# Kernel tuning notes

Hardware: AMD Instinct MI355X
Metric: run time of the kernel (lower is better)

The kernel has to match this reference:

```python
import jax, jax.numpy as jnp
import numpy as np

H, NH, L, S, B, V = 512, 8, 6, 2048, 2, 32000
DH = H // NH
EPS = 1e-5


def posenc(h, s):
    pos = jnp.arange(s, dtype=jnp.float32)[:, None]
    div = jnp.power(10000.0, jnp.arange(0, h, 2, dtype=jnp.float32) / h)
    pe = jnp.zeros((s, h), dtype=jnp.float32)
    pe = pe.at[:, 0::2].set(jnp.sin(pos / div))
    pe = pe.at[:, 1::2].set(jnp.cos(pos / div))
    return pe


def layernorm(x, g, b):
    mu = jnp.mean(x, axis=-1, keepdims=True)
    var = jnp.mean(jnp.square(x - mu), axis=-1, keepdims=True)
    return (x - mu) * jax.lax.rsqrt(var + EPS) * g + b


def setup_inputs() -> dict:
    key = jax.random.key(0)
    ks = jax.random.split(key, 16)
    sc = 0.02
    return {
        "src": jax.random.randint(ks[0], (B, S), 0, V),
        "mask": jnp.ones((B, 1, 1, S), dtype=jnp.int32),
        "emb": jax.random.normal(ks[1], (V, H), jnp.float32) * sc,
        "Wq": jax.random.normal(ks[2], (L, H, H), jnp.float32) * sc,
        "bq": jnp.zeros((L, H), jnp.float32),
        "Wk": jax.random.normal(ks[3], (L, H, H), jnp.float32) * sc,
        "bk": jnp.zeros((L, H), jnp.float32),
        "Wv": jax.random.normal(ks[4], (L, H, H), jnp.float32) * sc,
        "bv": jnp.zeros((L, H), jnp.float32),
        "Wo": jax.random.normal(ks[5], (L, H, H), jnp.float32) * sc,
        "bo": jnp.zeros((L, H), jnp.float32),
        "gamma": jnp.ones((L, H), jnp.float32),
        "beta": jnp.zeros((L, H), jnp.float32),
        "W1": jax.random.normal(ks[6], (L, H, 4 * H), jnp.float32) * sc,
        "b1": jnp.zeros((L, 4 * H), jnp.float32),
        "W2": jax.random.normal(ks[7], (L, 4 * H, H), jnp.float32) * sc,
        "b2": jnp.zeros((L, H), jnp.float32),
    }


def reference(src, mask, emb, Wq, bq, Wk, bk, Wv, bv, Wo, bo, gamma, beta, W1, b1, W2, b2):
    x = emb[src] + posenc(H, S)[None, :, :]  # [B,S,H]
    for i in range(L):
        q = (x @ Wq[i] + bq[i]).reshape(B, S, NH, DH).transpose(0, 2, 1, 3)
        k = (x @ Wk[i] + bk[i]).reshape(B, S, NH, DH).transpose(0, 2, 1, 3)
        v = (x @ Wv[i] + bv[i]).reshape(B, S, NH, DH).transpose(0, 2, 1, 3)
        scores = jnp.einsum("bhqd,bhkd->bhqk", q, k) / jnp.sqrt(jnp.float32(DH))
        scores = jnp.where(mask == 0, jnp.float32(-1e20), scores)
        attn = jax.nn.softmax(scores, axis=-1)
        av = jnp.einsum("bhqk,bhkd->bhqd", attn, v)
        attn_out = av.transpose(0, 2, 1, 3).reshape(B, S, H) @ Wo[i] + bo[i]
        # NOTE: same LayerNorm params applied to both sublayers (as in source)
        res = x + layernorm(attn_out, gamma[i], beta[i])
        ffn = jax.nn.relu(res @ W1[i] + b1[i]) @ W2[i] + b2[i]
        x = res + layernorm(ffn, gamma[i], beta[i])
    return x
```

## Files before the change

### kernel.cpp

```cpp
#include <hip/hip_runtime.h>
#include <math.h>

#define HDIM 512
#define NHEAD 8
#define NLAYER 6
#define SEQ 2048
#define BATCH 2
#define DHEAD 64
#define TOKENS (BATCH*SEQ)
#define FFND (4*HDIM)
#define QSTR 1536

typedef unsigned short u16;
typedef unsigned long long u64;
typedef __attribute__((ext_vector_type(8))) short short8;
typedef __attribute__((ext_vector_type(4))) float f32x4;

__device__ __forceinline__ u16 f2b(float f) {
  unsigned u = __float_as_uint(f);
  u += 0x7FFFu + ((u >> 16) & 1u);
  return (u16)(u >> 16);
}

__device__ __forceinline__ unsigned cvtpk_bf16(float lo, float hi) {
  unsigned r;
  asm("v_cvt_pk_bf16_f32 %0, %1, %2" : "=v"(r) : "v"(lo), "v"(hi));
  return r;
}

__device__ __forceinline__ void gload_lds16(const u16* g, u16* l) {
  __builtin_amdgcn_global_load_lds((const __attribute__((address_space(1))) void*)g,
                                   (__attribute__((address_space(3))) void*)l, 16, 0, 0);
}

__global__ void embed_pe(const int* __restrict__ src, const float* __restrict__ emb,
                         float* __restrict__ X, u16* __restrict__ Xb) {
  int tok = blockIdx.x;
  int lane = threadIdx.x;
  int s = tok & (SEQ - 1);
  int c0 = lane * 8;
  const float* e = emb + (long)src[tok] * HDIM + c0;
  float v[8];
#pragma unroll
  for (int j = 0; j < 8; j++) {
    int c = c0 + j;
    float arg = (float)s * exp2f(-(float)(c & ~1) * 0.02595256917f);
    v[j] = e[j] + ((c & 1) ? cosf(arg) : sinf(arg));
  }
  float* xp = X + (long)tok * HDIM + c0;
#pragma unroll
  for (int j = 0; j < 8; j++) xp[j] = v[j];
  u16 hb[8];
#pragma unroll
  for (int j = 0; j < 8; j++) hb[j] = f2b(v[j]);
  uint4 pk;
  pk.x = hb[0] | ((unsigned)hb[1] << 16);
  pk.y = hb[2] | ((unsigned)hb[3] << 16);
  pk.z = hb[4] | ((unsigned)hb[5] << 16);
  pk.w = hb[6] | ((unsigned)hb[7] << 16);
  *(uint4*)(Xb + (long)tok * HDIM + c0) = pk;
}

__global__ void maskprep(const int* __restrict__ mask, u64* __restrict__ mb) {
  int t = threadIdx.x;
  int b = t >> 5, tile = t & 31;
  const int* m = mask + b * SEQ + tile * 64;
  u64 w = 0;
#pragma unroll
  for (int j = 0; j < 64; j++) w |= (u64)(m[j] != 0) << j;
  mb[t] = w;
}

__global__ __launch_bounds__(256) void prep_weights(
    const float* __restrict__ Wq, const float* __restrict__ Wk, const float* __restrict__ Wv,
    const float* __restrict__ Wo, const float* __restrict__ W1, const float* __restrict__ W2,
    const float* __restrict__ bq, const float* __restrict__ bk, const float* __restrict__ bv,
    u16* __restrict__ Wqkvt, u16* __restrict__ Wot, u16* __restrict__ W1t, u16* __restrict__ W2t,
    float* __restrict__ bqkv) {
  int t = blockIdx.x;
  int tid = threadIdx.x;
  if (t == 768) {
    for (int i = tid; i < 1536; i += 256)
      bqkv[i] = (i < 512) ? bq[i] : (i < 1024) ? bk[i - 512] : bv[i - 1024];
    return;
  }
  const float* src; u16* dst; int K, N, kt, nt; long drow0 = 0;
  if (t < 192)      { int m = t / 64, r = t % 64; src = (m==0)?Wq:(m==1)?Wk:Wv; dst = Wqkvt; drow0 = (long)m*512; K=512;  N=512;  kt=r/8;  nt=r%8; }
  else if (t < 256) { int r = t - 192; src = Wo; dst = Wot; K=512;  N=512;  kt=r/8;  nt=r%8; }
  else if (t < 512) { int r = t - 256; src = W1; dst = W1t; K=512;  N=2048; kt=r/32; nt=r%32; }
  else              { int r = t - 512; src = W2; dst = W2t; K=2048; N=512;  kt=r/8;  nt=r%8; }
  __shared__ __align__(16) u16 Lt[64 * 72];
  int kl = tid >> 2;
#pragma unroll
  for (int rr = 0; rr < 4; rr++) {
    int cl = (tid & 3) * 4 + rr * 16;
    float4 v = *(const float4*)(src + (long)(kt * 64 + kl) * N + nt * 64 + cl);
    Lt[(cl + 0) * 72 + kl] = f2b(v.x);
    Lt[(cl + 1) * 72 + kl] = f2b(v.y);
    Lt[(cl + 2) * 72 + kl] = f2b(v.z);
    Lt[(cl + 3) * 72 + kl] = f2b(v.w);
  }
  __syncthreads();
  int nl = tid >> 2;
  int kc = (tid & 3) * 16;
  u16* dp = dst + (drow0 + nt * 64 + nl) * (long)K + kt * 64 + kc;
  *(uint4*)dp       = *(const uint4*)&Lt[nl * 72 + kc];
  *(uint4*)(dp + 8) = *(const uint4*)&Lt[nl * 72 + kc + 8];
}

__global__ __launch_bounds__(256) void vtranspose(const u16* __restrict__ QKV,
                                                  u16* __restrict__ Vtb) {
  __shared__ __align__(16) u16 Lt[64 * 72];
  int tid = threadIdx.x;
  int bh = blockIdx.y, b = bh >> 3, h = bh & 7;
  int s0 = blockIdx.x * 64;
  const u16* vsrc = QKV + (long)(b * SEQ + s0) * QSTR + 1024 + h * DHEAD;
  int key = tid >> 2, dc = (tid & 3) * 16;
  const u16* vp = vsrc + (long)key * QSTR + dc;
  uint4 v0 = *(const uint4*)vp;
  uint4 v1 = *(const uint4*)(vp + 8);
  unsigned vr[8] = { v0.x, v0.y, v0.z, v0.w, v1.x, v1.y, v1.z, v1.w };
#pragma unroll
  for (int j = 0; j < 8; j++) {
    Lt[(dc + 2 * j) * 72 + key]     = (u16)vr[j];
    Lt[(dc + 2 * j + 1) * 72 + key] = (u16)(vr[j] >> 16);
  }
  __syncthreads();
  int d = tid >> 2, kc = (tid & 3) * 16;
  u16* dst = Vtb + ((long)bh * DHEAD + d) * SEQ + s0 + kc;
  *(uint4*)dst       = *(const uint4*)&Lt[d * 72 + kc];
  *(uint4*)(dst + 8) = *(const uint4*)&Lt[d * 72 + kc + 8];
}

template <int BN, int KSPLIT, bool RELU, bool WF32, bool WB16>
__global__ __launch_bounds__(256) void gemm_tn(const u16* __restrict__ A,
                                               const u16* __restrict__ Bt,
                                               const float* __restrict__ bias,
                                               float* __restrict__ Cf,
                                               u16* __restrict__ Cb,
                                               int M, int N, int K) {
  constexpr int NF = BN / 32;
  __shared__ __align__(16) u16 As[2][128 * 32];
  __shared__ __align__(16) u16 Bs[2][BN * 32];
  int tid = threadIdx.x;
  int wave = tid >> 6, lane = tid & 63;
  int ln = lane & 15, hi = lane >> 4;
  int wm = wave >> 1, wn = wave & 1;
  int m0 = blockIdx.y * 128, n0 = blockIdx.x * BN;
  int z = (KSPLIT > 1) ? blockIdx.z : 0;
  int Ks = K / KSPLIT;
  const u16* Ab = A + z * Ks;
  const u16* Bb = Bt + z * Ks;

  f32x4 acc[4][NF] = {};

  int srow = lane >> 2;
  int skc  = (lane & 3) * 8;

  auto issue = [&](int kt, int buf) {
    int k0 = kt * 32;
#pragma unroll
    for (int j = 0; j < 2; j++) {
      int row = (wave * 2 + j) * 16 + srow;
      gload_lds16(Ab + (long)(m0 + row) * K + k0 + skc, &As[buf][row * 32 + skc]);
    }
#pragma unroll
    for (int j = 0; j < BN / 64; j++) {
      int row = (wave * (BN / 64) + j) * 16 + srow;
      gload_lds16(Bb + (long)(n0 + row) * K + k0 + skc, &Bs[buf][row * 32 + skc]);
    }
  };

  int NT = Ks / 32;
  issue(0, 0);
  __syncthreads();
  for (int kt = 0; kt < NT; kt++) {
    int buf = kt & 1;
    if (kt + 1 < NT) issue(kt + 1, buf ^ 1);
    short8 af[4], bf[NF];
#pragma unroll
    for (int mt = 0; mt < 4; mt++)
      af[mt] = *(const short8*)&As[buf][(wm * 64 + mt * 16 + ln) * 32 + 8 * hi];
#pragma unroll
    for (int nt = 0; nt < NF; nt++)
      bf[nt] = *(const short8*)&Bs[buf][(wn * (BN / 2) + nt * 16 + ln) * 32 + 8 * hi];
#pragma unroll
    for (int mt = 0; mt < 4; mt++)
#pragma unroll
      for (int nt = 0; nt < NF; nt++)
        acc[mt][nt] = __builtin_amdgcn_mfma_f32_16x16x32_bf16(af[mt], bf[nt], acc[mt][nt], 0, 0, 0);
    __syncthreads();
  }

  float* Cz = WF32 ? (Cf + (long)z * M * N) : nullptr;
#pragma unroll
  for (int mt = 0; mt < 4; mt++)
#pragma unroll
    for (int nt = 0; nt < NF; nt++)
#pragma unroll
      for (int r = 0; r < 4; r++) {
        int row = m0 + wm * 64 + mt * 16 + hi * 4 + r;
        int col = n0 + wn * (BN / 2) + nt * 16 + ln;
        float v = acc[mt][nt][r];
        if (KSPLIT == 1 || z == 0) v += bias[col];
        if (RELU) v = fmaxf(v, 0.0f);
        if (WF32) Cz[(long)row * N + col] = v;
        if (WB16) Cb[(long)row * N + col] = f2b(v);
      }
}

__global__ __launch_bounds__(256) void attention(const u16* __restrict__ QKV,
                                                 const u16* __restrict__ Vtb,
                                                 const u64* __restrict__ maskb,
                                                 u16* __restrict__ Og) {
  __shared__ __align__(16) u16 Ks[2][64 * 64];
  __shared__ __align__(16) u16 Vs[2][64 * 64];
  __shared__ u64 Msk[SEQ / 64];
  int tid = threadIdx.x, w = tid >> 6, lane = tid & 63;
  int ln = lane & 15, hi = lane >> 4;
  int h0 = hi & 1, h1 = hi >> 1, ln7 = ln & 7;
  int lin = blockIdx.x;
  int lid = (lin & 7) * 64 + (lin >> 3);
  int bh = lid >> 5, qt = lid & 31;
  int b = bh >> 3, h = bh & 7;
  int q0 = qt * 64 + w * 16;
  const u16* qbase = QKV + (long)b * SEQ * QSTR + h * DHEAD;
  const u16* kbase = qbase + 512;
  const u16* vtbase = Vtb + (long)bh * DHEAD * SEQ;

  short8 qf[2];
#pragma unroll
  for (int ks = 0; ks < 2; ks++)
    qf[ks] = *(const short8*)(qbase + (long)(q0 + ln) * QSTR + ks * 32 + 8 * hi);

  u64 mw0 = 0;
  if (tid < SEQ / 64) mw0 = maskb[b * (SEQ / 64) + tid];

  int sr0 = tid >> 3, sc = tid & 7;
  const u16 *kp0, *kp1, *vp0, *vp1;
  {
    int r1 = sr0 + 32;
    int key0 = (sr0 & 7) | ((sr0 & 0x18) << 1) | ((sr0 & 0x20) >> 2);
    int key1 = (r1 & 7) | ((r1 & 0x18) << 1) | ((r1 & 0x20) >> 2);
    kp0 = kbase + (long)key0 * QSTR + (sc ^ (sr0 & 7)) * 8;
    kp1 = kbase + (long)key1 * QSTR + (sc ^ (r1 & 7)) * 8;
    vp0 = vtbase + (long)sr0 * SEQ + (sc ^ (sr0 & 7)) * 8;
    vp1 = vtbase + (long)r1 * SEQ + (sc ^ (r1 & 7)) * 8;
  }
  int d0 = sr0 * 64 + sc * 8, d1 = d0 + 2048;

  auto issue = [&](int t, int buf) {
    long ko = (long)t * (64 * QSTR);
    int vo = t * 64;
    gload_lds16(kp0 + ko, &Ks[buf][d0]);
    gload_lds16(kp1 + ko, &Ks[buf][d1]);
    gload_lds16(vp0 + vo, &Vs[buf][d0]);
    gload_lds16(vp1 + vo, &Vs[buf][d1]);
  };

  f32x4 o[4] = {};
  float lsum = 0.0f;
  const int NT = SEQ / 64;

  issue(0, 0);
  issue(1, 1);
  if (tid < SEQ / 64) Msk[tid] = mw0;
  asm volatile("s_waitcnt vmcnt(4)" ::: "memory");
  __builtin_amdgcn_sched_barrier(0);
  __builtin_amdgcn_s_barrier();
  __builtin_amdgcn_sched_barrier(0);

  for (int t = 0; t < NT; t++) {
    int buf = t & 1;
    u64 mw = Msk[t];

    f32x4 s[4] = {};
#pragma unroll
    for (int ks = 0; ks < 2; ks++)
#pragma unroll
      for (int kb = 0; kb < 4; kb++) {
        short8 kf = *(const short8*)&Ks[buf][(kb * 16 + ln) * 64 + (((ks << 2) + hi) ^ ln7) * 8];
        s[kb] = __builtin_amdgcn_mfma_f32_16x16x32_bf16(kf, qf[ks], s[kb], 0, 0, 0);
      }

    unsigned D[4][2];
    if (mw == 0xFFFFFFFFFFFFFFFFull) {
#pragma unroll
      for (int kb = 0; kb < 4; kb++) {
        float p[4];
#pragma unroll
        for (int r = 0; r < 4; r++) {
          float pv = __expf(s[kb][r] * 0.125f);
          lsum += pv;
          p[r] = pv;
        }
        D[kb][0] = cvtpk_bf16(p[0], p[1]);
        D[kb][1] = cvtpk_bf16(p[2], p[3]);
      }
    } else {
      unsigned shb = h1 * 16 + h0 * 4;
      u64 mws = mw >> shb;
      unsigned nib[4] = { (unsigned)mws & 0xFu, (unsigned)(mws >> 32) & 0xFu,
                          (unsigned)(mws >> 8) & 0xFu, (unsigned)(mws >> 40) & 0xFu };
#pragma unroll
      for (int kb = 0; kb < 4; kb++) {
        float p[4];
#pragma unroll
        for (int r = 0; r < 4; r++) {
          float pv = __expf(s[kb][r] * 0.125f);
          pv = ((nib[kb] >> r) & 1u) ? pv : 0.0f;
          lsum += pv;
          p[r] = pv;
        }
        D[kb][0] = cvtpk_bf16(p[0], p[1]);
        D[kb][1] = cvtpk_bf16(p[2], p[3]);
      }
    }

    short8 pb[2];
#pragma unroll
    for (int ks = 0; ks < 2; ks++) {
      unsigned own0 = h0 ? D[2 + ks][0] : D[ks][0];
      unsigned own1 = h0 ? D[2 + ks][1] : D[ks][1];
      unsigned snd0 = h0 ? D[ks][0] : D[2 + ks][0];
      unsigned snd1 = h0 ? D[ks][1] : D[2 + ks][1];
      unsigned rc0 = (unsigned)__shfl_xor((int)snd0, 16);
      unsigned rc1 = (unsigned)__shfl_xor((int)snd1, 16);
      union { unsigned u[4]; short8 v; } pu;
      pu.u[0] = h0 ? rc0 : own0;
      pu.u[1] = h0 ? rc1 : own1;
      pu.u[2] = h0 ? own0 : rc0;
      pu.u[3] = h0 ? own1 : rc1;
      pb[ks] = pu.v;
    }

#pragma unroll
    for (int ks = 0; ks < 2; ks++)
#pragma unroll
      for (int mb = 0; mb < 4; mb++) {
        short8 vf = *(const short8*)&Vs[buf][(mb * 16 + ln) * 64 + (((ks << 2) + hi) ^ ln7) * 8];
        o[mb] = __builtin_amdgcn_mfma_f32_16x16x32_bf16(vf, pb[ks], o[mb], 0, 0, 0);
      }

    asm volatile("s_waitcnt lgkmcnt(0)" ::: "memory");
    __builtin_amdgcn_sched_barrier(0);
    __builtin_amdgcn_s_barrier();
    __builtin_amdgcn_sched_barrier(0);
    if (t + 2 < NT) {
      issue(t + 2, buf);
      asm volatile("s_waitcnt vmcnt(4)" ::: "memory");
    } else {
      asm volatile("s_waitcnt vmcnt(0)" ::: "memory");
    }
    __builtin_amdgcn_sched_barrier(0);
    __builtin_amdgcn_s_barrier();
    __builtin_amdgcn_sched_barrier(0);
  }

  lsum += __shfl_xor(lsum, 16);
  lsum += __shfl_xor(lsum, 32);
  float rl = 1.0f / lsum;

  u16* Ot = &Ks[0][0] + w * 1024;
#pragma unroll
  for (int mb = 0; mb < 4; mb++) {
    *(unsigned*)&Ot[ln * 64 + mb * 16 + hi * 4 + 0] = cvtpk_bf16(o[mb][0] * rl, o[mb][1] * rl);
    *(unsigned*)&Ot[ln * 64 + mb * 16 + hi * 4 + 2] = cvtpk_bf16(o[mb][2] * rl, o[mb][3] * rl);
  }
  asm volatile("s_waitcnt lgkmcnt(0)" ::: "memory");
  __builtin_amdgcn_s_barrier();
  u16* obase = Og + (long)b * SEQ * HDIM + h * DHEAD;
#pragma unroll
  for (int pass = 0; pass < 2; pass++) {
    int row = (lane >> 3) + 8 * pass;
    int c = lane & 7;
    uint4 val = *(const uint4*)&Ot[row * 64 + c * 8];
    *(uint4*)(obase + (long)(q0 + row) * HDIM + c * 8) = val;
  }
}

__global__ __launch_bounds__(256) void ln_residual(const float* __restrict__ Xin,
                                                   const float* __restrict__ T0,
                                                   const float* __restrict__ T1,
                                                   const float* __restrict__ gamma,
                                                   const float* __restrict__ beta,
                                                   float* __restrict__ Xout,
                                                   u16* __restrict__ Xb) {
  int tid = threadIdx.x, w = tid >> 6, lane = tid & 63;
  int row = blockIdx.x * 4 + w;
  const float* t0 = T0 + (long)row * HDIM;
  const float* t1 = T1 + (long)row * HDIM;
  int c0 = lane * 8;
  float v[8];
  {
    float4 a0 = *(const float4*)(t0 + c0);
    float4 b0 = *(const float4*)(t0 + c0 + 4);
    float4 a1 = *(const float4*)(t1 + c0);
    float4 b1 = *(const float4*)(t1 + c0 + 4);
    v[0] = a0.x + a1.x; v[1] = a0.y + a1.y; v[2] = a0.z + a1.z; v[3] = a0.w + a1.w;
    v[4] = b0.x + b1.x; v[5] = b0.y + b1.y; v[6] = b0.z + b1.z; v[7] = b0.w + b1.w;
  }
  float sum = 0.0f;
#pragma unroll
  for (int j = 0; j < 8; j++) sum += v[j];
#pragma unroll
  for (int off = 32; off; off >>= 1) sum += __shfl_xor(sum, off);
  float mu = sum * (1.0f / HDIM);
  float sq = 0.0f;
#pragma unroll
  for (int j = 0; j < 8; j++) { float d = v[j] - mu; sq += d * d; }
#pragma unroll
  for (int off = 32; off; off >>= 1) sq += __shfl_xor(sq, off);
  float rs = rsqrtf(sq * (1.0f / HDIM) + 1e-5f);
  const float* xin = Xin + (long)row * HDIM + c0;
  float* xout = Xout + (long)row * HDIM + c0;
  u16 hb[8];
#pragma unroll
  for (int j = 0; j < 8; j++) {
    int c = c0 + j;
    float y = xin[j] + (v[j] - mu) * rs * gamma[c] + beta[c];
    xout[j] = y;
    hb[j] = f2b(y);
  }
  uint4 pk;
  pk.x = hb[0] | ((unsigned)hb[1] << 16);
  pk.y = hb[2] | ((unsigned)hb[3] << 16);
  pk.z = hb[4] | ((unsigned)hb[5] << 16);
  pk.w = hb[6] | ((unsigned)hb[7] << 16);
  *(uint4*)(Xb + (long)row * HDIM + c0) = pk;
}

extern "C" void kernel_launch(void* const* d_in, const int* in_sizes, int n_in,
                              void* d_out, int out_size, void* d_ws, size_t ws_size,
                              hipStream_t stream) {
  const int*   src   = (const int*)d_in[0];
  const int*   mask  = (const int*)d_in[1];
  const float* emb   = (const float*)d_in[2];
  const float* Wq    = (const float*)d_in[3];
  const float* bq    = (const float*)d_in[4];
  const float* Wk    = (const float*)d_in[5];
  const float* bk    = (const float*)d_in[6];
  const float* Wv    = (const float*)d_in[7];
  const float* bv    = (const float*)d_in[8];
  const float* Wo    = (const float*)d_in[9];
  const float* bo    = (const float*)d_in[10];
  const float* gamma = (const float*)d_in[11];
  const float* beta  = (const float*)d_in[12];
  const float* W1    = (const float*)d_in[13];
  const float* b1    = (const float*)d_in[14];
  const float* W2    = (const float*)d_in[15];
  const float* b2    = (const float*)d_in[16];

  char* ws = (char*)d_ws;
  float* X     = (float*)(ws);
  u16*   Xb    = (u16*)(ws + (8ll << 20));
  u16*   QKVb  = (u16*)(ws + (12ll << 20));
  u16*   Mb    = (u16*)(ws + (12ll << 20));
  u16*   AVb   = (u16*)(ws + (24ll << 20));
  float* T     = (float*)(ws + (28ll << 20));
  u16*   Wqkvt = (u16*)(ws + (44ll << 20));
  u16*   Wot   = (u16*)(ws + (45ll << 20) + (512ll << 10));
  u16*   W1t   = (u16*)(ws + (46ll << 20));
  u16*   W2t   = (u16*)(ws + (48ll << 20));
  float* bqkv  = (float*)(ws + (50ll << 20));
  u16*   Vtb   = (u16*)(ws + (51ll << 20));
  u64*   maskbits = (u64*)(ws + (55ll << 20));
  float* T1    = T + (long)TOKENS * HDIM;

  embed_pe<<<dim3(TOKENS), dim3(64), 0, stream>>>(src, emb, X, Xb);
  maskprep<<<dim3(1), dim3(64), 0, stream>>>(mask, maskbits);

  for (int i = 0; i < NLAYER; i++) {
    long wo = (long)i * HDIM * HDIM;
    prep_weights<<<dim3(769), 256, 0, stream>>>(
        Wq + wo, Wk + wo, Wv + wo, Wo + wo,
        W1 + (long)i * HDIM * FFND, W2 + (long)i * FFND * HDIM,
        bq + i * HDIM, bk + i * HDIM, bv + i * HDIM,
        Wqkvt, Wot, W1t, W2t, bqkv);

    gemm_tn<128, 1, false, false, true><<<dim3(QSTR / 128, TOKENS / 128), 256, 0, stream>>>(
        Xb, Wqkvt, bqkv, nullptr, QKVb, TOKENS, QSTR, HDIM);

    vtranspose<<<dim3(SEQ / 64, BATCH * NHEAD), 256, 0, stream>>>(QKVb, Vtb);

    attention<<<dim3(512), 256, 0, stream>>>(QKVb, Vtb, maskbits, AVb);

    gemm_tn<64, 2, false, true, false><<<dim3(HDIM / 64, TOKENS / 128, 2), 256, 0, stream>>>(
        AVb, Wot, bo + i * HDIM, T, nullptr, TOKENS, HDIM, HDIM);

    ln_residual<<<dim3(TOKENS / 4), 256, 0, stream>>>(X, T, T1, gamma + i * HDIM,
                                                      beta + i * HDIM, X, Xb);

    gemm_tn<128, 1, true, false, true><<<dim3(FFND / 128, TOKENS / 128), 256, 0, stream>>>(
        Xb, W1t, b1 + (long)i * FFND, nullptr, Mb, TOKENS, FFND, HDIM);

    gemm_tn<64, 2, false, true, false><<<dim3(HDIM / 64, TOKENS / 128, 2), 256, 0, stream>>>(
        Mb, W2t, b2 + i * HDIM, T, nullptr, TOKENS, HDIM, FFND);

    ln_residual<<<dim3(TOKENS / 4), 256, 0, stream>>>(X, T, T1, gamma + i * HDIM,
                                                      beta + i * HDIM, X, Xb);
  }

  hipMemcpyAsync(d_out, X, (size_t)TOKENS * HDIM * sizeof(float),
                 hipMemcpyDeviceToDevice, stream);
}
```

Measured before the change: 1.012 ms.

## Split attention over two key halves and merge partials in separate kernel

Attention now runs 1024 blocks, each handling half of the key sequence, and writes unnormalized fp32 partial outputs and row sums to workspace. A new attn_merge kernel adds the two partials, normalizes them and writes the bf16 output. The aim is to raise parallelism on a GPU with many CUs, where 512 blocks underfill the device. In exchange it adds an extra launch and fp32 partial traffic. The merge relies on the base kernel's softmax having no running max, so the partials can be summed directly.

Measured after the change: 998.7 us. About the same (-1.3%).

```diff
diff --git a/kernel.cpp b/kernel.cpp
--- a/kernel.cpp
+++ b/kernel.cpp
@@ -212,7 +212,8 @@
 __global__ __launch_bounds__(256) void attention(const u16* __restrict__ QKV,
                                                  const u16* __restrict__ Vtb,
                                                  const u64* __restrict__ maskb,
-                                                 u16* __restrict__ Og) {
+                                                 float* __restrict__ Opart,
+                                                 float* __restrict__ Lpart) {
   __shared__ __align__(16) u16 Ks[2][64 * 64];
   __shared__ __align__(16) u16 Vs[2][64 * 64];
   __shared__ u64 Msk[SEQ / 64];
@@ -220,8 +221,8 @@
   int ln = lane & 15, hi = lane >> 4;
   int h0 = hi & 1, h1 = hi >> 1, ln7 = ln & 7;
   int lin = blockIdx.x;
-  int lid = (lin & 7) * 64 + (lin >> 3);
-  int bh = lid >> 5, qt = lid & 31;
+  int lid = (lin & 7) * 128 + (lin >> 3);
+  int bh = lid >> 6, qt = (lid >> 1) & 31, kz = lid & 1;
   int b = bh >> 3, h = bh & 7;
   int q0 = qt * 64 + w * 16;
   const u16* qbase = QKV + (long)b * SEQ * QSTR + h * DHEAD;
@@ -260,19 +261,20 @@
 
   f32x4 o[4] = {};
   float lsum = 0.0f;
-  const int NT = SEQ / 64;
-
-  issue(0, 0);
-  issue(1, 1);
+  const int t0 = kz * 16;
+  const int NTL = 16;
+
+  issue(t0, 0);
+  issue(t0 + 1, 1);
   if (tid < SEQ / 64) Msk[tid] = mw0;
   asm volatile("s_waitcnt vmcnt(4)" ::: "memory");
   __builtin_amdgcn_sched_barrier(0);
   __builtin_amdgcn_s_barrier();
   __builtin_amdgcn_sched_barrier(0);
 
-  for (int t = 0; t < NT; t++) {
-    int buf = t & 1;
-    u64 mw = Msk[t];
+  for (int ti = 0; ti < NTL; ti++) {
+    int buf = ti & 1;
+    u64 mw = Msk[t0 + ti];
 
     f32x4 s[4] = {};
 #pragma unroll
@@ -346,8 +348,8 @@
     __builtin_amdgcn_sched_barrier(0);
     __builtin_amdgcn_s_barrier();
     __builtin_amdgcn_sched_barrier(0);
-    if (t + 2 < NT) {
-      issue(t + 2, buf);
+    if (ti + 2 < NTL) {
+      issue(t0 + ti + 2, buf);
       asm volatile("s_waitcnt vmcnt(4)" ::: "memory");
     } else {
       asm volatile("s_waitcnt vmcnt(0)" ::: "memory");
@@ -359,23 +361,39 @@
 
   lsum += __shfl_xor(lsum, 16);
   lsum += __shfl_xor(lsum, 32);
-  float rl = 1.0f / lsum;
-
-  u16* Ot = &Ks[0][0] + w * 1024;
-#pragma unroll
-  for (int mb = 0; mb < 4; mb++) {
-    *(unsigned*)&Ot[ln * 64 + mb * 16 + hi * 4 + 0] = cvtpk_bf16(o[mb][0] * rl, o[mb][1] * rl);
-    *(unsigned*)&Ot[ln * 64 + mb * 16 + hi * 4 + 2] = cvtpk_bf16(o[mb][2] * rl, o[mb][3] * rl);
-  }
-  asm volatile("s_waitcnt lgkmcnt(0)" ::: "memory");
-  __builtin_amdgcn_s_barrier();
-  u16* obase = Og + (long)b * SEQ * HDIM + h * DHEAD;
-#pragma unroll
-  for (int pass = 0; pass < 2; pass++) {
-    int row = (lane >> 3) + 8 * pass;
-    int c = lane & 7;
-    uint4 val = *(const uint4*)&Ot[row * 64 + c * 8];
-    *(uint4*)(obase + (long)(q0 + row) * HDIM + c * 8) = val;
+
+  float* OpB = Opart + (long)lid * 4096 + w * 1024;
+#pragma unroll
+  for (int mb = 0; mb < 4; mb++)
+    *(f32x4*)&OpB[ln * 64 + mb * 16 + hi * 4] = o[mb];
+  if (hi == 0) Lpart[(long)lid * 64 + w * 16 + ln] = lsum;
+}
+
+__global__ __launch_bounds__(256) void attn_merge(const float* __restrict__ Op,
+                                                  const float* __restrict__ Lp,
+                                                  u16* __restrict__ Og) {
+  int lin = blockIdx.x;
+  int mlid = (lin & 7) * 64 + (lin >> 3);
+  int bh = mlid >> 5, qt = mlid & 31;
+  int b = bh >> 3, h = bh & 7;
+  int tid = threadIdx.x;
+  __shared__ float Ls[64];
+  if (tid < 64) Ls[tid] = 1.0f / (Lp[(long)mlid * 128 + tid] + Lp[(long)mlid * 128 + 64 + tid]);
+  __syncthreads();
+  const float* P0 = Op + (long)mlid * 8192;
+  const float* P1 = P0 + 4096;
+  u16* obase = Og + (long)b * SEQ * HDIM + (long)qt * 64 * HDIM + h * DHEAD;
+#pragma unroll
+  for (int j = 0; j < 4; j++) {
+    int flat = j * 1024 + tid * 4;
+    int row = flat >> 6, c = flat & 63;
+    float4 a = *(const float4*)&P0[flat];
+    float4 bb = *(const float4*)&P1[flat];
+    float rl = Ls[row];
+    uint2 val;
+    val.x = cvtpk_bf16((a.x + bb.x) * rl, (a.y + bb.y) * rl);
+    val.y = cvtpk_bf16((a.z + bb.z) * rl, (a.w + bb.w) * rl);
+    *(uint2*)(obase + (long)row * HDIM + c) = val;
   }
 }
 
@@ -463,8 +481,10 @@
   u16*   W1t   = (u16*)(ws + (46ll << 20));
   u16*   W2t   = (u16*)(ws + (48ll << 20));
   float* bqkv  = (float*)(ws + (50ll << 20));
+  float* Lpart = (float*)(ws + (50ll << 20) + (512ll << 10));
   u16*   Vtb   = (u16*)(ws + (51ll << 20));
   u64*   maskbits = (u64*)(ws + (55ll << 20));
+  float* Opart = T;
   float* T1    = T + (long)TOKENS * HDIM;
 
   embed_pe<<<dim3(TOKENS), dim3(64), 0, stream>>>(src, emb, X, Xb);
@@ -483,7 +503,9 @@
 
     vtranspose<<<dim3(SEQ / 64, BATCH * NHEAD), 256, 0, stream>>>(QKVb, Vtb);
 
-    attention<<<dim3(512), 256, 0, stream>>>(QKVb, Vtb, maskbits, AVb);
+    attention<<<dim3(1024), 256, 0, stream>>>(QKVb, Vtb, maskbits, Opart, Lpart);
+
+    attn_merge<<<dim3(512), 256, 0, stream>>>(Opart, Lpart, AVb);
 
     gemm_tn<64, 2, false, true, false><<<dim3(HDIM / 64, TOKENS / 128, 2), 256, 0, stream>>>(
         AVb, Wot, bo + i * HDIM, T, nullptr, TOKENS, HDIM, HDIM);
```
